# Performance work log

Hardware: AMD Instinct MI355X
Metric: run time of the kernel (lower is better)

## Reference

```python
import jax, jax.numpy as jnp
import numpy as np

B, T, D = 2, 2048, 2048
N, K, H = 16, 8, 128  # num_heads, num_kv_heads, head_dim
SOFTCAP = 50.0
ROPE_BASE = 10000.0


def apply_rope(x, positions):
    # x: [B, L, heads, H], positions: [B, L]
    head_dim = x.shape[-1]
    fraction = 2.0 * jnp.arange(head_dim // 2, dtype=jnp.float32) / head_dim
    timescale = ROPE_BASE ** fraction  # [H/2]
    sinusoid = positions.astype(jnp.float32)[..., None] / timescale  # [B, L, H/2]
    sinusoid = sinusoid[..., None, :]  # [B, L, 1, H/2]
    sin, cos = jnp.sin(sinusoid), jnp.cos(sinusoid)
    first, second = jnp.split(x, 2, axis=-1)
    out = jnp.concatenate([first * cos - second * sin,
                           second * cos + first * sin], axis=-1)
    return out.astype(x.dtype)


def setup_inputs() -> dict:
    key = jax.random.key(0)
    kx, kq, kkv, ko = jax.random.split(key, 4)
    x = jax.random.normal(kx, (B, T, D), dtype=jnp.float32)
    positions = jnp.broadcast_to(jnp.arange(T, dtype=jnp.int32), (B, T))
    attn_mask = jnp.broadcast_to(
        jnp.tril(jnp.ones((T, T), dtype=bool))[None, None], (B, 1, T, T))
    # variance-scaling fan_in init approximated with scaled normals
    w_q = jax.random.normal(kq, (N, D, H), dtype=jnp.float32) / np.sqrt(D)
    w_kv = jax.random.normal(kkv, (2, K, D, H), dtype=jnp.float32) / np.sqrt(D)
    w_out = jax.random.normal(ko, (N, H, D), dtype=jnp.float32) / np.sqrt(N * H)
    return {"x": x, "positions": positions, "attn_mask": attn_mask,
            "w_q": w_q, "w_kv": w_kv, "w_out": w_out}


def reference(x, positions, attn_mask, w_q, w_kv, w_out):
    # QKV projections (GQA: separate q and kv einsums)
    q = jnp.einsum('BTD,NDH->BTNH', x, w_q)        # [B,T,N,H]
    kv = jnp.einsum('BSD,cKDH->cBSKH', x, w_kv)     # [2,B,S,K,H]
    k, v = kv[0], kv[1]
    q = apply_rope(q, positions) * (H ** -0.5)      # rsqrt_head_dim norm
    k = apply_rope(k, positions)
    # GQA grouping: N = K * G
    G = N // K
    qg = q.reshape(B, T, K, G, H)
    logits = jnp.einsum('BTKGH,BSKH->BKGTS', qg, k).astype(jnp.float32)
    logits = jnp.tanh(logits / SOFTCAP) * SOFTCAP   # logits softcap
    big_neg = -2.3819763e+38
    masked = jnp.where(attn_mask[:, :, None, :, :], logits, big_neg)
    probs = jax.nn.softmax(masked, axis=-1).astype(k.dtype)
    encoded = jnp.einsum('BKGTS,BSKH->BTKGH', probs, v).reshape(B, T, N, H)
    return jnp.einsum('BTNH,NHD->BTD', encoded, w_out)
```

## Files before the change

### kernel.cpp

```cpp
#include <hip/hip_runtime.h>
#include <math.h>
#include <stdint.h>


typedef unsigned short u16;
using bf16x8 = __attribute__((ext_vector_type(8))) short;
using f32x4  = __attribute__((ext_vector_type(4))) float;

#define MFMA_BF16(a,b,c) __builtin_amdgcn_mfma_f32_16x16x32_bf16((a),(b),(c),0,0,0)

static __device__ __forceinline__ float b2f(u16 u) {
  union { unsigned int i; float f; } v; v.i = ((unsigned int)u) << 16; return v.f;
}
static __device__ __forceinline__ u16 f2b(float f) {
  union { float f; unsigned int i; } v; v.f = f;
  unsigned int r = v.i + 0x7fffu + ((v.i >> 16) & 1u);
  return (u16)(r >> 16);
}
static __device__ __forceinline__ unsigned pk2(float x0, float x1) {
  union { float f; unsigned u; } a, b;
  a.f = x0; b.f = x1;
  return __builtin_amdgcn_perm(b.u + 0x8000u, a.u + 0x8000u, 0x07060302u);
}
static __device__ __forceinline__ float rexp2(float a) {
  float r;
  asm("v_exp_f32 %0, %1" : "=v"(r) : "v"(a));
  return r;
}
static __device__ __forceinline__ void gload_lds16(const void* g, void* l) {
  __builtin_amdgcn_global_load_lds((__attribute__((address_space(1))) void*)(g),
                                   (__attribute__((address_space(3))) void*)(l),
                                   16, 0, 0);
}

__global__ __launch_bounds__(256) void prep(const float* __restrict__ x, u16* __restrict__ xb,
                                            const float* __restrict__ wq,
                                            const float* __restrict__ wkv,
                                            const float* __restrict__ wout,
                                            u16* __restrict__ wqkvt, u16* __restrict__ woutt) {
  const int tid = threadIdx.x;
  int bid = blockIdx.x;
  if (bid < 8192) {
    const int i = (bid * 256 + tid) * 4;
    const float4 v = *(const float4*)(x + i);
    ushort4 o;
    o.x = f2b(v.x); o.y = f2b(v.y); o.z = f2b(v.z); o.w = f2b(v.w);
    *(ushort4*)(xb + i) = o;
    return;
  }
  bid -= 8192;
  const float* src;
  u16* dst;
  int rows, cols, bx, by;
  if (bid < 8192) {
    const int seg = bid >> 12;
    const int r = bid & 4095;
    const int mat = r >> 8;
    bx = (r & 255) & 3;
    by = (r & 255) >> 2;
    rows = 2048; cols = 128;
    src = (seg ? wkv : wq) + (size_t)mat * 2048 * 128;
    dst = wqkvt + (size_t)(seg * 16 + mat) * 2048 * 128;
  } else {
    const int r = bid - 8192;
    bx = r & 63;
    by = r >> 6;
    rows = 2048; cols = 2048;
    src = wout;
    dst = woutt;
  }
  __shared__ u16 tile[32][33];
  const int c0 = bx * 32, r0 = by * 32;
  const int tx = tid & 31, ty = tid >> 5;
#pragma unroll
  for (int j = 0; j < 4; ++j)
    tile[ty + j * 8][tx] = f2b(src[(size_t)(r0 + ty + j * 8) * cols + (c0 + tx)]);
  __syncthreads();
#pragma unroll
  for (int j = 0; j < 4; ++j)
    dst[(size_t)(c0 + ty + j * 8) * rows + (r0 + tx)] = tile[tx][ty + j * 8];
}

__global__ __launch_bounds__(512, 2) void gemm_qkv(const u16* __restrict__ X,
                                                   const u16* __restrict__ wqkvt,
                                                   u16* __restrict__ qb,
                                                   u16* __restrict__ kb,
                                                   u16* __restrict__ vtb) {
  __shared__ __align__(16) u16 sAB[2][2][16384];
  const int m0 = blockIdx.x * 256;
  const int ct0 = blockIdx.y * 2;
  const u16* BT = wqkvt + (size_t)blockIdx.y * 256 * 2048;
  const int tid = threadIdx.x;
  const int wave = tid >> 6, lane = tid & 63;
  const int wm = wave >> 2, wn = wave & 3;
  const int quad = lane >> 4, l16 = lane & 15;
  const int srow = lane >> 3;
  const int sch = (lane & 7) ^ srow;

  f32x4 acc[8][4] = {};

  auto STAGE = [&](int kt, int bsel) {
    const int k0 = kt * 64;
#pragma unroll
    for (int s = 0; s < 4; ++s) {
      const int ia = wave * 4 + s;
      const int row = ia * 8 + srow;
      gload_lds16(X + (size_t)(m0 + row) * 2048 + k0 + sch * 8,
                  (char*)&sAB[bsel][0][0] + ia * 1024);
      gload_lds16(BT + (size_t)row * 2048 + k0 + sch * 8,
                  (char*)&sAB[bsel][1][0] + ia * 1024);
    }
  };

  auto COMPUTE = [&](int bsel) {
    const char* aB = (const char*)&sAB[bsel][0][0];
    const char* bB = (const char*)&sAB[bsel][1][0];
#pragma unroll
    for (int ks = 0; ks < 2; ++ks) {
      bf16x8 bfr[4];
#pragma unroll
      for (int nf = 0; nf < 4; ++nf) {
        const int Rb = wn * 64 + nf * 16 + l16;
        bfr[nf] = *(const bf16x8*)(bB + Rb * 128 + (((ks * 4 + quad) ^ (Rb & 7)) << 4));
      }
      __builtin_amdgcn_s_setprio(1);
#pragma unroll
      for (int mf = 0; mf < 8; ++mf) {
        const int R = wm * 128 + mf * 16 + l16;
        const bf16x8 af = *(const bf16x8*)(aB + R * 128 + (((ks * 4 + quad) ^ (R & 7)) << 4));
#pragma unroll
        for (int nf = 0; nf < 4; ++nf)
          acc[mf][nf] = MFMA_BF16(af, bfr[nf], acc[mf][nf]);
      }
      __builtin_amdgcn_s_setprio(0);
    }
  };

  STAGE(0, 0);
#pragma unroll 1
  for (int t = 0; t < 31; ++t) {
    STAGE(t + 1, (t + 1) & 1);
    asm volatile("s_waitcnt vmcnt(8)" ::: "memory");
    __builtin_amdgcn_s_barrier();
    asm volatile("" ::: "memory");
    COMPUTE(t & 1);
    asm volatile("" ::: "memory");
    __builtin_amdgcn_s_barrier();
    asm volatile("" ::: "memory");
  }
  asm volatile("s_waitcnt vmcnt(0)" ::: "memory");
  __builtin_amdgcn_s_barrier();
  asm volatile("" ::: "memory");
  COMPUTE(1);

#pragma unroll
  for (int mf = 0; mf < 8; ++mf) {
    const int mm = m0 + wm * 128 + mf * 16 + quad * 4;
    const int b = mm >> 11;
    const int t = mm & 2047;
#pragma unroll
    for (int nf = 0; nf < 4; ++nf) {
      const int colg = wn * 64 + nf * 16;
      const int ct = ct0 + (colg >> 7);
      const int h = (colg & 127) + l16;
      if (ct < 16) {
        u16* d = qb + (((size_t)b * 16 + ct) * 2048 + t) * 128 + h;
#pragma unroll
        for (int i = 0; i < 4; ++i) d[(size_t)i * 128] = f2b(acc[mf][nf][i]);
      } else if (ct < 24) {
        u16* d = kb + (((size_t)b * 8 + (ct - 16)) * 2048 + t) * 128 + h;
#pragma unroll
        for (int i = 0; i < 4; ++i) d[(size_t)i * 128] = f2b(acc[mf][nf][i]);
      } else {
        u16* d = vtb + (((size_t)b * 8 + (ct - 24)) * 128 + h) * 2048 + t;
        uint2 pkv;
        pkv.x = (unsigned)f2b(acc[mf][nf][0]) | ((unsigned)f2b(acc[mf][nf][1]) << 16);
        pkv.y = (unsigned)f2b(acc[mf][nf][2]) | ((unsigned)f2b(acc[mf][nf][3]) << 16);
        *(uint2*)d = pkv;
      }
    }
  }
}

__global__ __launch_bounds__(256) void rope_kernel(u16* __restrict__ qb,
                                                   u16* __restrict__ kb,
                                                   const int* __restrict__ pos) {
  const unsigned idx = blockIdx.x * 256 + threadIdx.x;
  const unsigned QP = 1u << 21;
  u16* p;
  float scale;
  int b, t, j2;
  if (idx < QP) {
    j2 = (int)(idx & 31) * 2; t = (int)((idx >> 5) & 2047);
    const int hd = (int)((idx >> 16) & 15); b = (int)(idx >> 20);
    p = qb + (((size_t)b * 16 + hd) * 2048 + t) * 128;
    scale = 0.08838834764831845f;
  } else {
    const unsigned r = idx - QP;
    j2 = (int)(r & 31) * 2; t = (int)((r >> 5) & 2047);
    const int hd = (int)((r >> 16) & 7); b = (int)(r >> 19);
    p = kb + (((size_t)b * 8 + hd) * 2048 + t) * 128;
    scale = 1.0f;
  }
  const float fpos = (float)pos[(size_t)b * 2048 + t];
  const unsigned lo = *(const unsigned*)(p + j2);
  const unsigned hi = *(const unsigned*)(p + j2 + 64);
  unsigned olo = 0, ohi = 0;
#pragma unroll
  for (int d = 0; d < 2; ++d) {
    const int j = j2 + d;
    const float ang = fpos * exp2f((float)j * -0.2076205059304601f);
    float sn, cs;
    sincosf(ang, &sn, &cs);
    const float a = b2f((u16)((d ? (lo >> 16) : lo) & 0xffffu));
    const float c2 = b2f((u16)((d ? (hi >> 16) : hi) & 0xffffu));
    olo |= ((unsigned)f2b((a * cs - c2 * sn) * scale)) << (16 * d);
    ohi |= ((unsigned)f2b((c2 * cs + a * sn) * scale)) << (16 * d);
  }
  *(unsigned*)(p + j2) = olo;
  *(unsigned*)(p + j2 + 64) = ohi;
}

__global__ __launch_bounds__(256, 4) void attn_fused(const u16* __restrict__ qg,
                                                     const u16* __restrict__ kg,
                                                     const u16* __restrict__ vtg,
                                                     u16* __restrict__ enc) {
  __shared__ __align__(16) char lds[32768];
  char* sK = lds;
  char* sV = lds + 16384;

  const int bid = blockIdx.x;
  const int half = bid >> 9;
  const int r = bid & 511;
  const int x = r & 7;
  const int g = r >> 3;
  const int pr = g & 15;
  const int head = (g >> 4) * 8 + x;
  const int Q = half ? pr : (31 - pr);
  const int b = head >> 4;
  const int n = head & 15;
  const int kh = n >> 1;

  const u16* qbase = qg + ((size_t)b * 16 + n) * 2048 * 128;
  const u16* kbase = kg + ((size_t)b * 8 + kh) * 2048 * 128;
  const u16* vbase = vtg + ((size_t)b * 8 + kh) * 128 * 2048;

  const int tid = threadIdx.x, wave = tid >> 6, lane = tid & 63;
  const int quad = lane >> 4, l16 = lane & 15;
  const int bp_a0 = ((quad & 1) * 32 + l16) * 4;
  const int bp_a1 = bp_a0 + 64;

  const float L2E = 1.4426950408889634f;
  const float C50 = 72.13475204444817f;
  const float B1 = 1.9235933879e-4f;
  const float B2 = 3.0777494206e-8f;
  const float B3 = 4.9830224200e-12f;

  const u16* kp[4];
  const u16* vp[4];
#pragma unroll
  for (int s = 0; s < 4; ++s) {
    const int kr = wave * 16 + s * 4 + quad;
    kp[s] = kbase + (size_t)kr * 128 + (l16 ^ (s * 4 + quad)) * 8;
    const int vr = wave * 32 + s * 8 + (lane >> 3);
    vp[s] = vbase + (size_t)vr * 2048 + ((lane & 7) ^ (lane >> 3)) * 8;
  }

  const int tw = Q * 64 + wave * 16;
  const int tlane = tw + l16;

  bf16x8 qf[4];
#pragma unroll
  for (int kf = 0; kf < 4; ++kf)
    qf[kf] = *(const bf16x8*)(qbase + (size_t)tlane * 128 + kf * 32 + quad * 8);

  f32x4 o[8] = {};
  f32x4 lacc = {0.f, 0.f, 0.f, 0.f};

#pragma unroll
  for (int s = 0; s < 4; ++s) {
    gload_lds16(kp[s], sK + (wave * 4 + s) * 1024);
    kp[s] += 64 * 128;
  }
#pragma unroll
  for (int s = 0; s < 4; ++s) {
    gload_lds16(vp[s], sV + (wave * 4 + s) * 1024);
    vp[s] += 64;
  }

#pragma unroll 1
  for (int si = 0; si <= Q; ++si) {
    const int s0 = si * 64;
    asm volatile("s_waitcnt vmcnt(4)" ::: "memory");
    __builtin_amdgcn_s_barrier();
    asm volatile("" ::: "memory");

    const bool diag = (si == Q);
    const int nfmax = diag ? wave : 3;
    const int kmax = diag ? (wave >> 1) : 1;

    f32x4 sacc[4];
    __builtin_amdgcn_s_setprio(1);
#pragma unroll
    for (int nf = 0; nf < 4; ++nf) {
      if (nf <= nfmax) {
        const int sr = nf * 16 + l16;
        f32x4 a = {0.f, 0.f, 0.f, 0.f};
#pragma unroll
        for (int kf = 0; kf < 4; ++kf) {
          const bf16x8 kfr =
              *(const bf16x8*)(sK + sr * 256 + (((kf * 4 + quad) ^ (sr & 15)) << 4));
          a = MFMA_BF16(kfr, qf[kf], a);
        }
        sacc[nf] = a;
      }
    }
    __builtin_amdgcn_s_setprio(0);

    asm volatile("" ::: "memory");
    __builtin_amdgcn_s_barrier();
    asm volatile("" ::: "memory");
    if (si < Q) {
#pragma unroll
      for (int s = 0; s < 4; ++s) {
        gload_lds16(kp[s], sK + (wave * 4 + s) * 1024);
        kp[s] += 64 * 128;
      }
    }

#pragma unroll
    for (int nf = 0; nf < 4; ++nf) {
      if (nf <= nfmax) {
        const f32x4 xv = sacc[nf];
        const f32x4 u = xv * xv;
        f32x4 t = u * (-B3) + B2;
        t = u * t + (-B1);
        t = u * t + L2E;
        f32x4 pv;
#pragma unroll
        for (int i = 0; i < 4; ++i) pv[i] = rexp2(fmaf(xv[i], t[i], -C50));
        if (diag) {
#pragma unroll
          for (int i = 0; i < 4; ++i) {
            const int sg = s0 + nf * 16 + quad * 4 + i;
            if (sg > tlane) pv[i] = 0.0f;
          }
        }
        sacc[nf] = pv;
        lacc += pv;
      }
    }

    unsigned pkd[4][2];
#pragma unroll
    for (int nf = 0; nf < 4; ++nf) {
      if (nf <= nfmax) {
        pkd[nf][0] = pk2(sacc[nf][0], sacc[nf][1]);
        pkd[nf][1] = pk2(sacc[nf][2], sacc[nf][3]);
      } else {
        pkd[nf][0] = 0u; pkd[nf][1] = 0u;
      }
    }

    union { int d[4]; bf16x8 v; } pb[2];
#pragma unroll
    for (int c2 = 0; c2 < 2; ++c2) {
      if (c2 <= kmax) {
        const int lo = (quad >> 1);
        const int dA0 = __builtin_amdgcn_ds_bpermute(bp_a0, (int)pkd[2 * c2][0]);
        const int dB0 = __builtin_amdgcn_ds_bpermute(bp_a0, (int)pkd[2 * c2 + 1][0]);
        const int dA1 = __builtin_amdgcn_ds_bpermute(bp_a0, (int)pkd[2 * c2][1]);
        const int dB1 = __builtin_amdgcn_ds_bpermute(bp_a0, (int)pkd[2 * c2 + 1][1]);
        const int dA2 = __builtin_amdgcn_ds_bpermute(bp_a1, (int)pkd[2 * c2][0]);
        const int dB2 = __builtin_amdgcn_ds_bpermute(bp_a1, (int)pkd[2 * c2 + 1][0]);
        const int dA3 = __builtin_amdgcn_ds_bpermute(bp_a1, (int)pkd[2 * c2][1]);
        const int dB3 = __builtin_amdgcn_ds_bpermute(bp_a1, (int)pkd[2 * c2 + 1][1]);
        pb[c2].d[0] = lo ? dB0 : dA0;
        pb[c2].d[1] = lo ? dB1 : dA1;
        pb[c2].d[2] = lo ? dB2 : dA2;
        pb[c2].d[3] = lo ? dB3 : dA3;
      }
    }

    if (si < Q) {
      asm volatile("s_waitcnt vmcnt(4)" ::: "memory");
    } else {
      asm volatile("s_waitcnt vmcnt(0)" ::: "memory");
    }
    __builtin_amdgcn_s_barrier();
    asm volatile("" ::: "memory");

#pragma unroll
    for (int c2 = 0; c2 < 2; ++c2) {
      if (c2 <= kmax) {
        __builtin_amdgcn_s_setprio(1);
#pragma unroll
        for (int nfo = 0; nfo < 8; ++nfo) {
          const int hr = nfo * 16 + l16;
          const bf16x8 vb =
              *(const bf16x8*)(sV + hr * 128 + (((c2 * 4 + quad) ^ (hr & 7)) << 4));
          o[nfo] = MFMA_BF16(vb, pb[c2].v, o[nfo]);
        }
        __builtin_amdgcn_s_setprio(0);
      }
    }

    asm volatile("" ::: "memory");
    __builtin_amdgcn_s_barrier();
    asm volatile("" ::: "memory");
    if (si < Q) {
#pragma unroll
      for (int s = 0; s < 4; ++s) {
        gload_lds16(vp[s], sV + (wave * 4 + s) * 1024);
        vp[s] += 64;
      }
    }
  }

  float lsum = lacc[0] + lacc[1] + lacc[2] + lacc[3];
  lsum += __shfl_xor(lsum, 16);
  lsum += __shfl_xor(lsum, 32);
  const float inv = 1.0f / lsum;
  u16* d = enc + (((size_t)b * 2048 + tlane) * 16 + n) * 128 + quad * 4;
#pragma unroll
  for (int nfo = 0; nfo < 8; ++nfo) {
    uint2 st;
    st.x = (unsigned)f2b(o[nfo][0] * inv) | ((unsigned)f2b(o[nfo][1] * inv) << 16);
    st.y = (unsigned)f2b(o[nfo][2] * inv) | ((unsigned)f2b(o[nfo][3] * inv) << 16);
    *(uint2*)(d + nfo * 16) = st;
  }
}

__global__ __launch_bounds__(512, 2) void gemm_out(const u16* __restrict__ A,
                                                   const u16* __restrict__ Bt,
                                                   float* __restrict__ C) {
  __shared__ __align__(16) u16 sA[2][16384];
  __shared__ __align__(16) u16 sB[2][8192];
  const int m0 = blockIdx.x * 256;
  const int n0 = blockIdx.y * 128;
  const int tid = threadIdx.x;
  const int wave = tid >> 6, lane = tid & 63;
  const int wm = wave >> 2, wn = wave & 3;
  const int quad = lane >> 4, l16 = lane & 15;
  const int srow = lane >> 3;
  const int sch = (lane & 7) ^ srow;

  f32x4 acc[8][2] = {};

  auto STAGE = [&](int kt, int bsel) {
    const int k0 = kt * 64;
#pragma unroll
    for (int s = 0; s < 4; ++s) {
      const int ia = wave * 4 + s;
      const int row = ia * 8 + srow;
      gload_lds16(A + (size_t)(m0 + row) * 2048 + k0 + sch * 8,
                  (char*)&sA[bsel][0] + ia * 1024);
    }
#pragma unroll
    for (int s = 0; s < 2; ++s) {
      const int ib = wave * 2 + s;
      const int row = ib * 8 + srow;
      gload_lds16(Bt + (size_t)(n0 + row) * 2048 + k0 + sch * 8,
                  (char*)&sB[bsel][0] + ib * 1024);
    }
  };

  auto COMPUTE = [&](int bsel) {
    const char* aB = (const char*)&sA[bsel][0];
    const char* bB = (const char*)&sB[bsel][0];
#pragma unroll
    for (int ks = 0; ks < 2; ++ks) {
      bf16x8 bfr[2];
#pragma unroll
      for (int nf = 0; nf < 2; ++nf) {
        const int Rb = wn * 32 + nf * 16 + l16;
        bfr[nf] = *(const bf16x8*)(bB + Rb * 128 + (((ks * 4 + quad) ^ (Rb & 7)) << 4));
      }
      __builtin_amdgcn_s_setprio(1);
#pragma unroll
      for (int mf = 0; mf < 8; ++mf) {
        const int R = wm * 128 + mf * 16 + l16;
        const bf16x8 af = *(const bf16x8*)(aB + R * 128 + (((ks * 4 + quad) ^ (R & 7)) << 4));
#pragma unroll
        for (int nf = 0; nf < 2; ++nf)
          acc[mf][nf] = MFMA_BF16(af, bfr[nf], acc[mf][nf]);
      }
      __builtin_amdgcn_s_setprio(0);
    }
  };

  STAGE(0, 0);
#pragma unroll 1
  for (int t = 0; t < 31; ++t) {
    STAGE(t + 1, (t + 1) & 1);
    asm volatile("s_waitcnt vmcnt(6)" ::: "memory");
    __builtin_amdgcn_s_barrier();
    asm volatile("" ::: "memory");
    COMPUTE(t & 1);
    asm volatile("" ::: "memory");
    __builtin_amdgcn_s_barrier();
    asm volatile("" ::: "memory");
  }
  asm volatile("s_waitcnt vmcnt(0)" ::: "memory");
  __builtin_amdgcn_s_barrier();
  asm volatile("" ::: "memory");
  COMPUTE(1);

#pragma unroll
  for (int mf = 0; mf < 8; ++mf) {
    const int mm = m0 + wm * 128 + mf * 16 + quad * 4;
#pragma unroll
    for (int nf = 0; nf < 2; ++nf) {
      const int col = n0 + wn * 32 + nf * 16 + l16;
#pragma unroll
      for (int i = 0; i < 4; ++i) C[(size_t)(mm + i) * 2048 + col] = acc[mf][nf][i];
    }
  }
}

extern "C" void kernel_launch(void* const* d_in, const int* in_sizes, int n_in,
                              void* d_out, int out_size, void* d_ws, size_t ws_size,
                              hipStream_t stream) {
  (void)in_sizes; (void)n_in; (void)out_size; (void)ws_size;
  const float* x     = (const float*)d_in[0];
  const int*   posi  = (const int*)d_in[1];
  const float* w_q   = (const float*)d_in[3];
  const float* w_kv  = (const float*)d_in[4];
  const float* w_out = (const float*)d_in[5];
  float* out = (float*)d_out;

  u16* ws = (u16*)d_ws;
  u16* wqkvt = ws;
  u16* woutt = ws + (size_t)8388608;
  u16* qb    = ws + (size_t)12582912;
  u16* kb    = ws + (size_t)20971520;
  u16* vtb   = ws + (size_t)25165824;
  u16* encb  = ws + (size_t)29360128;
  u16* xb    = encb;

  prep<<<20480, 256, 0, stream>>>(x, xb, w_q, w_kv, w_out, wqkvt, woutt);
  gemm_qkv<<<dim3(16, 16), 512, 0, stream>>>(xb, wqkvt, qb, kb, vtb);
  rope_kernel<<<12288, 256, 0, stream>>>(qb, kb, posi);
  attn_fused<<<1024, 256, 0, stream>>>(qb, kb, vtb, encb);
  gemm_out<<<dim3(16, 16), 512, 0, stream>>>(encb, woutt, out);
}
```

Before: 334.2 us.

## Double attention tile to 128 queries and 128 keys with 8-wave blocks

The attention kernel now uses 512-thread blocks covering 128 query rows and 128-key tiles, with 64 KB of LDS, and launches half as many blocks. Each K/V tile staged in LDS is shared by twice as many query rows, and there are half as many barrier-separated iterations per block. The softmax exponent and packing are interleaved with the QK MFMAs in two halves. In exchange it risks lower occupancy from the larger LDS and register footprint, more wasted work on the diagonal tile, and fewer blocks for load balancing.

```diff
diff --git a/kernel.cpp b/kernel.cpp
--- a/kernel.cpp
+++ b/kernel.cpp
@@ -221,22 +221,22 @@
   *(unsigned*)(p + j2 + 64) = ohi;
 }
 
-__global__ __launch_bounds__(256, 4) void attn_fused(const u16* __restrict__ qg,
+__global__ __launch_bounds__(512, 4) void attn_fused(const u16* __restrict__ qg,
                                                      const u16* __restrict__ kg,
                                                      const u16* __restrict__ vtg,
                                                      u16* __restrict__ enc) {
-  __shared__ __align__(16) char lds[32768];
+  __shared__ __align__(16) char lds[65536];
   char* sK = lds;
-  char* sV = lds + 16384;
+  char* sV = lds + 32768;
 
   const int bid = blockIdx.x;
-  const int half = bid >> 9;
-  const int r = bid & 511;
+  const int half = bid >> 8;
+  const int r = bid & 255;
   const int x = r & 7;
   const int g = r >> 3;
-  const int pr = g & 15;
-  const int head = (g >> 4) * 8 + x;
-  const int Q = half ? pr : (31 - pr);
+  const int pr = g & 7;
+  const int head = (g >> 3) * 8 + x;
+  const int Q = half ? pr : (15 - pr);
   const int b = head >> 4;
   const int n = head & 15;
   const int kh = n >> 1;
@@ -260,13 +260,13 @@
   const u16* vp[4];
 #pragma unroll
   for (int s = 0; s < 4; ++s) {
-    const int kr = wave * 16 + s * 4 + quad;
-    kp[s] = kbase + (size_t)kr * 128 + (l16 ^ (s * 4 + quad)) * 8;
-    const int vr = wave * 32 + s * 8 + (lane >> 3);
-    vp[s] = vbase + (size_t)vr * 2048 + ((lane & 7) ^ (lane >> 3)) * 8;
-  }
-
-  const int tw = Q * 64 + wave * 16;
+    const int row = wave * 16 + s * 4 + quad;
+    const int ch = l16 ^ (row & 15);
+    kp[s] = kbase + (size_t)row * 128 + ch * 8;
+    vp[s] = vbase + (size_t)row * 2048 + ch * 8;
+  }
+
+  const int tw = Q * 128 + wave * 16;
   const int tlane = tw + l16;
 
   bf16x8 qf[4];
@@ -280,42 +280,74 @@
 #pragma unroll
   for (int s = 0; s < 4; ++s) {
     gload_lds16(kp[s], sK + (wave * 4 + s) * 1024);
-    kp[s] += 64 * 128;
+    kp[s] += 128 * 128;
   }
 #pragma unroll
   for (int s = 0; s < 4; ++s) {
     gload_lds16(vp[s], sV + (wave * 4 + s) * 1024);
-    vp[s] += 64;
+    vp[s] += 128;
   }
 
 #pragma unroll 1
   for (int si = 0; si <= Q; ++si) {
-    const int s0 = si * 64;
+    const int s0 = si * 128;
     asm volatile("s_waitcnt vmcnt(4)" ::: "memory");
     __builtin_amdgcn_s_barrier();
     asm volatile("" ::: "memory");
 
     const bool diag = (si == Q);
-    const int nfmax = diag ? wave : 3;
-    const int kmax = diag ? (wave >> 1) : 1;
-
-    f32x4 sacc[4];
-    __builtin_amdgcn_s_setprio(1);
-#pragma unroll
-    for (int nf = 0; nf < 4; ++nf) {
-      if (nf <= nfmax) {
-        const int sr = nf * 16 + l16;
-        f32x4 a = {0.f, 0.f, 0.f, 0.f};
-#pragma unroll
-        for (int kf = 0; kf < 4; ++kf) {
-          const bf16x8 kfr =
-              *(const bf16x8*)(sK + sr * 256 + (((kf * 4 + quad) ^ (sr & 15)) << 4));
-          a = MFMA_BF16(kfr, qf[kf], a);
+    const int nfmax = diag ? wave : 7;
+    const int kmax = diag ? (wave >> 1) : 3;
+
+    unsigned pkd[8][2];
+#pragma unroll
+    for (int hh = 0; hh < 2; ++hh) {
+      f32x4 sacc[4];
+      __builtin_amdgcn_s_setprio(1);
+#pragma unroll
+      for (int j = 0; j < 4; ++j) {
+        const int nf = hh * 4 + j;
+        if (nf <= nfmax) {
+          const int sr = nf * 16 + l16;
+          f32x4 a = {0.f, 0.f, 0.f, 0.f};
+#pragma unroll
+          for (int kf = 0; kf < 4; ++kf) {
+            const bf16x8 kfr =
+                *(const bf16x8*)(sK + sr * 256 + (((kf * 4 + quad) ^ (sr & 15)) << 4));
+            a = MFMA_BF16(kfr, qf[kf], a);
+          }
+          sacc[j] = a;
         }
-        sacc[nf] = a;
-      }
-    }
-    __builtin_amdgcn_s_setprio(0);
+      }
+      __builtin_amdgcn_s_setprio(0);
+
+#pragma unroll
+      for (int j = 0; j < 4; ++j) {
+        const int nf = hh * 4 + j;
+        if (nf <= nfmax) {
+          const f32x4 xv = sacc[j];
+          const f32x4 u = xv * xv;
+          f32x4 t = u * (-B3) + B2;
+          t = u * t + (-B1);
+          t = u * t + L2E;
+          f32x4 pv;
+#pragma unroll
+          for (int i = 0; i < 4; ++i) pv[i] = rexp2(fmaf(xv[i], t[i], -C50));
+          if (diag) {
+#pragma unroll
+            for (int i = 0; i < 4; ++i) {
+              const int sg = s0 + nf * 16 + quad * 4 + i;
+              if (sg > tlane) pv[i] = 0.0f;
+            }
+          }
+          lacc += pv;
+          pkd[nf][0] = pk2(pv[0], pv[1]);
+          pkd[nf][1] = pk2(pv[2], pv[3]);
+        } else {
+          pkd[nf][0] = 0u; pkd[nf][1] = 0u;
+        }
+      }
+    }
 
     asm volatile("" ::: "memory");
     __builtin_amdgcn_s_barrier();
@@ -324,47 +356,20 @@
 #pragma unroll
       for (int s = 0; s < 4; ++s) {
         gload_lds16(kp[s], sK + (wave * 4 + s) * 1024);
-        kp[s] += 64 * 128;
-      }
-    }
-
-#pragma unroll
-    for (int nf = 0; nf < 4; ++nf) {
-      if (nf <= nfmax) {
-        const f32x4 xv = sacc[nf];
-        const f32x4 u = xv * xv;
-        f32x4 t = u * (-B3) + B2;
-        t = u * t + (-B1);
-        t = u * t + L2E;
-        f32x4 pv;
-#pragma unroll
-        for (int i = 0; i < 4; ++i) pv[i] = rexp2(fmaf(xv[i], t[i], -C50));
-        if (diag) {
-#pragma unroll
-          for (int i = 0; i < 4; ++i) {
-            const int sg = s0 + nf * 16 + quad * 4 + i;
-            if (sg > tlane) pv[i] = 0.0f;
-          }
-        }
-        sacc[nf] = pv;
-        lacc += pv;
-      }
-    }
-
-    unsigned pkd[4][2];
-#pragma unroll
-    for (int nf = 0; nf < 4; ++nf) {
-      if (nf <= nfmax) {
-        pkd[nf][0] = pk2(sacc[nf][0], sacc[nf][1]);
-        pkd[nf][1] = pk2(sacc[nf][2], sacc[nf][3]);
-      } else {
-        pkd[nf][0] = 0u; pkd[nf][1] = 0u;
-      }
-    }
-
-    union { int d[4]; bf16x8 v; } pb[2];
-#pragma unroll
-    for (int c2 = 0; c2 < 2; ++c2) {
+        kp[s] += 128 * 128;
+      }
+    }
+
+    if (si < Q) {
+      asm volatile("s_waitcnt vmcnt(4)" ::: "memory");
+    } else {
+      asm volatile("s_waitcnt vmcnt(0)" ::: "memory");
+    }
+    __builtin_amdgcn_s_barrier();
+    asm volatile("" ::: "memory");
+
+#pragma unroll
+    for (int c2 = 0; c2 < 4; ++c2) {
       if (c2 <= kmax) {
         const int lo = (quad >> 1);
         const int dA0 = __builtin_amdgcn_ds_bpermute(bp_a0, (int)pkd[2 * c2][0]);
@@ -375,31 +380,18 @@
         const int dB2 = __builtin_amdgcn_ds_bpermute(bp_a1, (int)pkd[2 * c2 + 1][0]);
         const int dA3 = __builtin_amdgcn_ds_bpermute(bp_a1, (int)pkd[2 * c2][1]);
         const int dB3 = __builtin_amdgcn_ds_bpermute(bp_a1, (int)pkd[2 * c2 + 1][1]);
-        pb[c2].d[0] = lo ? dB0 : dA0;
-        pb[c2].d[1] = lo ? dB1 : dA1;
-        pb[c2].d[2] = lo ? dB2 : dA2;
-        pb[c2].d[3] = lo ? dB3 : dA3;
-      }
-    }
-
-    if (si < Q) {
-      asm volatile("s_waitcnt vmcnt(4)" ::: "memory");
-    } else {
-      asm volatile("s_waitcnt vmcnt(0)" ::: "memory");
-    }
-    __builtin_amdgcn_s_barrier();
-    asm volatile("" ::: "memory");
-
-#pragma unroll
-    for (int c2 = 0; c2 < 2; ++c2) {
-      if (c2 <= kmax) {
+        union { int d[4]; bf16x8 v; } pb;
+        pb.d[0] = lo ? dB0 : dA0;
+        pb.d[1] = lo ? dB1 : dA1;
+        pb.d[2] = lo ? dB2 : dA2;
+        pb.d[3] = lo ? dB3 : dA3;
         __builtin_amdgcn_s_setprio(1);
 #pragma unroll
         for (int nfo = 0; nfo < 8; ++nfo) {
           const int hr = nfo * 16 + l16;
           const bf16x8 vb =
-              *(const bf16x8*)(sV + hr * 128 + (((c2 * 4 + quad) ^ (hr & 7)) << 4));
-          o[nfo] = MFMA_BF16(vb, pb[c2].v, o[nfo]);
+              *(const bf16x8*)(sV + hr * 256 + (((c2 * 4 + quad) ^ (hr & 15)) << 4));
+          o[nfo] = MFMA_BF16(vb, pb.v, o[nfo]);
         }
         __builtin_amdgcn_s_setprio(0);
       }
@@ -412,7 +404,7 @@
 #pragma unroll
       for (int s = 0; s < 4; ++s) {
         gload_lds16(vp[s], sV + (wave * 4 + s) * 1024);
-        vp[s] += 64;
+        vp[s] += 128;
       }
     }
   }
@@ -541,6 +533,6 @@
   prep<<<20480, 256, 0, stream>>>(x, xb, w_q, w_kv, w_out, wqkvt, woutt);
   gemm_qkv<<<dim3(16, 16), 512, 0, stream>>>(xb, wqkvt, qb, kb, vtb);
   rope_kernel<<<12288, 256, 0, stream>>>(qb, kb, posi);
-  attn_fused<<<1024, 256, 0, stream>>>(qb, kb, vtb, encb);
+  attn_fused<<<512, 512, 0, stream>>>(qb, kb, vtb, encb);
   gemm_out<<<dim3(16, 16), 512, 0, stream>>>(encb, woutt, out);
 }
```

After: 336.0 us. Within noise of the previous version (+0.6%).

## Split attention key tile across wave pairs with two query groups per wave

Applied to the files above, without the earlier changes.

Reassigns work inside the attention block so each wave handles 32 query rows (two 16-row groups) against half of the 64-key tile, rather than 16 query rows against all keys. Each loaded K and V fragment now feeds two MFMAs, which halves LDS reads per MFMA and doubles reuse. Waves whose key half lies fully above the causal diagonal skip work. Partial outputs and row sums from the two key halves are combined through LDS at the end, which adds an epilogue reduction and raises register pressure from doubled accumulators.

```diff
diff --git a/kernel.cpp b/kernel.cpp
--- a/kernel.cpp
+++ b/kernel.cpp
@@ -246,6 +246,7 @@
   const u16* vbase = vtg + ((size_t)b * 8 + kh) * 128 * 2048;
 
   const int tid = threadIdx.x, wave = tid >> 6, lane = tid & 63;
+  const int tslot = wave & 1, shalf = wave >> 1;
   const int quad = lane >> 4, l16 = lane & 15;
   const int bp_a0 = ((quad & 1) * 32 + l16) * 4;
   const int bp_a1 = bp_a0 + 64;
@@ -266,16 +267,18 @@
     vp[s] = vbase + (size_t)vr * 2048 + ((lane & 7) ^ (lane >> 3)) * 8;
   }
 
-  const int tw = Q * 64 + wave * 16;
-  const int tlane = tw + l16;
-
-  bf16x8 qf[4];
-#pragma unroll
-  for (int kf = 0; kf < 4; ++kf)
-    qf[kf] = *(const bf16x8*)(qbase + (size_t)tlane * 128 + kf * 32 + quad * 8);
-
-  f32x4 o[8] = {};
-  f32x4 lacc = {0.f, 0.f, 0.f, 0.f};
+  const int tw = Q * 64 + tslot * 32;
+
+  bf16x8 qf[2][4];
+#pragma unroll
+  for (int gg = 0; gg < 2; ++gg)
+#pragma unroll
+    for (int kf = 0; kf < 4; ++kf)
+      qf[gg][kf] = *(const bf16x8*)(qbase + (size_t)(tw + gg * 16 + l16) * 128 + kf * 32 + quad * 8);
+
+  f32x4 o[2][8] = {};
+  f32x4 lacc0 = {0.f, 0.f, 0.f, 0.f};
+  f32x4 lacc1 = {0.f, 0.f, 0.f, 0.f};
 
 #pragma unroll
   for (int s = 0; s < 4; ++s) {
@@ -290,32 +293,35 @@
 
 #pragma unroll 1
   for (int si = 0; si <= Q; ++si) {
-    const int s0 = si * 64;
+    const int s0w = si * 64 + shalf * 32;
+    const int dl = tw + 31 - s0w;
+    const bool live = dl >= 0;
+    const bool dodiag = (s0w + 31 > tw);
+
     asm volatile("s_waitcnt vmcnt(4)" ::: "memory");
     __builtin_amdgcn_s_barrier();
     asm volatile("" ::: "memory");
 
-    const bool diag = (si == Q);
-    const int nfmax = diag ? wave : 3;
-    const int kmax = diag ? (wave >> 1) : 1;
-
-    f32x4 sacc[4];
-    __builtin_amdgcn_s_setprio(1);
-#pragma unroll
-    for (int nf = 0; nf < 4; ++nf) {
-      if (nf <= nfmax) {
-        const int sr = nf * 16 + l16;
-        f32x4 a = {0.f, 0.f, 0.f, 0.f};
+    f32x4 sa[2][2];
+    if (live) {
+      __builtin_amdgcn_s_setprio(1);
+#pragma unroll
+      for (int nf = 0; nf < 2; ++nf) {
+        const int sr = shalf * 32 + nf * 16 + l16;
+        f32x4 a0 = {0.f, 0.f, 0.f, 0.f};
+        f32x4 a1 = {0.f, 0.f, 0.f, 0.f};
 #pragma unroll
         for (int kf = 0; kf < 4; ++kf) {
           const bf16x8 kfr =
               *(const bf16x8*)(sK + sr * 256 + (((kf * 4 + quad) ^ (sr & 15)) << 4));
-          a = MFMA_BF16(kfr, qf[kf], a);
+          a0 = MFMA_BF16(kfr, qf[0][kf], a0);
+          a1 = MFMA_BF16(kfr, qf[1][kf], a1);
         }
-        sacc[nf] = a;
-      }
-    }
-    __builtin_amdgcn_s_setprio(0);
+        sa[nf][0] = a0;
+        sa[nf][1] = a1;
+      }
+      __builtin_amdgcn_s_setprio(0);
+    }
 
     asm volatile("" ::: "memory");
     __builtin_amdgcn_s_barrier();
@@ -328,57 +334,52 @@
       }
     }
 
-#pragma unroll
-    for (int nf = 0; nf < 4; ++nf) {
-      if (nf <= nfmax) {
-        const f32x4 xv = sacc[nf];
-        const f32x4 u = xv * xv;
-        f32x4 t = u * (-B3) + B2;
-        t = u * t + (-B1);
-        t = u * t + L2E;
-        f32x4 pv;
-#pragma unroll
-        for (int i = 0; i < 4; ++i) pv[i] = rexp2(fmaf(xv[i], t[i], -C50));
-        if (diag) {
-#pragma unroll
-          for (int i = 0; i < 4; ++i) {
-            const int sg = s0 + nf * 16 + quad * 4 + i;
-            if (sg > tlane) pv[i] = 0.0f;
+    unsigned pkd[2][2][2];
+    if (live) {
+#pragma unroll
+      for (int nf = 0; nf < 2; ++nf) {
+#pragma unroll
+        for (int gg = 0; gg < 2; ++gg) {
+          const f32x4 xv = sa[nf][gg];
+          const f32x4 u = xv * xv;
+          f32x4 t = u * (-B3) + B2;
+          t = u * t + (-B1);
+          t = u * t + L2E;
+          f32x4 pv;
+#pragma unroll
+          for (int i = 0; i < 4; ++i) pv[i] = rexp2(fmaf(xv[i], t[i], -C50));
+          if (dodiag) {
+            const int tl = tw + gg * 16 + l16;
+#pragma unroll
+            for (int i = 0; i < 4; ++i) {
+              const int sg = s0w + nf * 16 + quad * 4 + i;
+              if (sg > tl) pv[i] = 0.0f;
+            }
           }
+          if (gg == 0) lacc0 += pv; else lacc1 += pv;
+          pkd[gg][nf][0] = pk2(pv[0], pv[1]);
+          pkd[gg][nf][1] = pk2(pv[2], pv[3]);
         }
-        sacc[nf] = pv;
-        lacc += pv;
-      }
-    }
-
-    unsigned pkd[4][2];
-#pragma unroll
-    for (int nf = 0; nf < 4; ++nf) {
-      if (nf <= nfmax) {
-        pkd[nf][0] = pk2(sacc[nf][0], sacc[nf][1]);
-        pkd[nf][1] = pk2(sacc[nf][2], sacc[nf][3]);
-      } else {
-        pkd[nf][0] = 0u; pkd[nf][1] = 0u;
       }
     }
 
     union { int d[4]; bf16x8 v; } pb[2];
-#pragma unroll
-    for (int c2 = 0; c2 < 2; ++c2) {
-      if (c2 <= kmax) {
-        const int lo = (quad >> 1);
-        const int dA0 = __builtin_amdgcn_ds_bpermute(bp_a0, (int)pkd[2 * c2][0]);
-        const int dB0 = __builtin_amdgcn_ds_bpermute(bp_a0, (int)pkd[2 * c2 + 1][0]);
-        const int dA1 = __builtin_amdgcn_ds_bpermute(bp_a0, (int)pkd[2 * c2][1]);
-        const int dB1 = __builtin_amdgcn_ds_bpermute(bp_a0, (int)pkd[2 * c2 + 1][1]);
-        const int dA2 = __builtin_amdgcn_ds_bpermute(bp_a1, (int)pkd[2 * c2][0]);
-        const int dB2 = __builtin_amdgcn_ds_bpermute(bp_a1, (int)pkd[2 * c2 + 1][0]);
-        const int dA3 = __builtin_amdgcn_ds_bpermute(bp_a1, (int)pkd[2 * c2][1]);
-        const int dB3 = __builtin_amdgcn_ds_bpermute(bp_a1, (int)pkd[2 * c2 + 1][1]);
-        pb[c2].d[0] = lo ? dB0 : dA0;
-        pb[c2].d[1] = lo ? dB1 : dA1;
-        pb[c2].d[2] = lo ? dB2 : dA2;
-        pb[c2].d[3] = lo ? dB3 : dA3;
+    if (live) {
+      const int lo = (quad >> 1);
+#pragma unroll
+      for (int gg = 0; gg < 2; ++gg) {
+        const int dA0 = __builtin_amdgcn_ds_bpermute(bp_a0, (int)pkd[gg][0][0]);
+        const int dB0 = __builtin_amdgcn_ds_bpermute(bp_a0, (int)pkd[gg][1][0]);
+        const int dA1 = __builtin_amdgcn_ds_bpermute(bp_a0, (int)pkd[gg][0][1]);
+        const int dB1 = __builtin_amdgcn_ds_bpermute(bp_a0, (int)pkd[gg][1][1]);
+        const int dA2 = __builtin_amdgcn_ds_bpermute(bp_a1, (int)pkd[gg][0][0]);
+        const int dB2 = __builtin_amdgcn_ds_bpermute(bp_a1, (int)pkd[gg][1][0]);
+        const int dA3 = __builtin_amdgcn_ds_bpermute(bp_a1, (int)pkd[gg][0][1]);
+        const int dB3 = __builtin_amdgcn_ds_bpermute(bp_a1, (int)pkd[gg][1][1]);
+        pb[gg].d[0] = lo ? dB0 : dA0;
+        pb[gg].d[1] = lo ? dB1 : dA1;
+        pb[gg].d[2] = lo ? dB2 : dA2;
+        pb[gg].d[3] = lo ? dB3 : dA3;
       }
     }
 
@@ -390,19 +391,17 @@
     __builtin_amdgcn_s_barrier();
     asm volatile("" ::: "memory");
 
-#pragma unroll
-    for (int c2 = 0; c2 < 2; ++c2) {
-      if (c2 <= kmax) {
-        __builtin_amdgcn_s_setprio(1);
-#pragma unroll
-        for (int nfo = 0; nfo < 8; ++nfo) {
-          const int hr = nfo * 16 + l16;
-          const bf16x8 vb =
-              *(const bf16x8*)(sV + hr * 128 + (((c2 * 4 + quad) ^ (hr & 7)) << 4));
-          o[nfo] = MFMA_BF16(vb, pb[c2].v, o[nfo]);
-        }
-        __builtin_amdgcn_s_setprio(0);
-      }
+    if (live) {
+      __builtin_amdgcn_s_setprio(1);
+#pragma unroll
+      for (int nfo = 0; nfo < 8; ++nfo) {
+        const int hr = nfo * 16 + l16;
+        const bf16x8 vb =
+            *(const bf16x8*)(sV + hr * 128 + (((shalf * 4 + quad) ^ (hr & 7)) << 4));
+        o[0][nfo] = MFMA_BF16(vb, pb[0].v, o[0][nfo]);
+        o[1][nfo] = MFMA_BF16(vb, pb[1].v, o[1][nfo]);
+      }
+      __builtin_amdgcn_s_setprio(0);
     }
 
     asm volatile("" ::: "memory");
@@ -417,17 +416,46 @@
     }
   }
 
-  float lsum = lacc[0] + lacc[1] + lacc[2] + lacc[3];
-  lsum += __shfl_xor(lsum, 16);
-  lsum += __shfl_xor(lsum, 32);
-  const float inv = 1.0f / lsum;
-  u16* d = enc + (((size_t)b * 2048 + tlane) * 16 + n) * 128 + quad * 4;
-#pragma unroll
-  for (int nfo = 0; nfo < 8; ++nfo) {
-    uint2 st;
-    st.x = (unsigned)f2b(o[nfo][0] * inv) | ((unsigned)f2b(o[nfo][1] * inv) << 16);
-    st.y = (unsigned)f2b(o[nfo][2] * inv) | ((unsigned)f2b(o[nfo][3] * inv) << 16);
-    *(uint2*)(d + nfo * 16) = st;
+  float lsum0 = lacc0[0] + lacc0[1] + lacc0[2] + lacc0[3];
+  lsum0 += __shfl_xor(lsum0, 16); lsum0 += __shfl_xor(lsum0, 32);
+  float lsum1 = lacc1[0] + lacc1[1] + lacc1[2] + lacc1[3];
+  lsum1 += __shfl_xor(lsum1, 16); lsum1 += __shfl_xor(lsum1, 32);
+
+  float* red = (float*)lds;
+  __syncthreads();
+  if (lane < 16) {
+    red[(wave * 2 + 0) * 16 + lane] = lsum0;
+    red[(wave * 2 + 1) * 16 + lane] = lsum1;
+  }
+  __syncthreads();
+  const int pw = wave ^ 2;
+  lsum0 += red[(pw * 2 + 0) * 16 + l16];
+  lsum1 += red[(pw * 2 + 1) * 16 + l16];
+  __syncthreads();
+  if (shalf) {
+#pragma unroll
+    for (int gg = 0; gg < 2; ++gg)
+#pragma unroll
+      for (int nfo = 0; nfo < 8; ++nfo)
+        *(f32x4*)(lds + (((tslot * 2 + gg) * 8 + nfo) * 1024) + lane * 16) = o[gg][nfo];
+  }
+  __syncthreads();
+  if (!shalf) {
+#pragma unroll
+    for (int gg = 0; gg < 2; ++gg) {
+      const float inv = 1.0f / (gg ? lsum1 : lsum0);
+      const int tlg = tw + gg * 16 + l16;
+      u16* d = enc + (((size_t)b * 2048 + tlg) * 16 + n) * 128 + quad * 4;
+#pragma unroll
+      for (int nfo = 0; nfo < 8; ++nfo) {
+        f32x4 ov = o[gg][nfo];
+        ov += *(const f32x4*)(lds + (((tslot * 2 + gg) * 8 + nfo) * 1024) + lane * 16);
+        uint2 st;
+        st.x = (unsigned)f2b(ov[0] * inv) | ((unsigned)f2b(ov[1] * inv) << 16);
+        st.y = (unsigned)f2b(ov[2] * inv) | ((unsigned)f2b(ov[3] * inv) << 16);
+        *(uint2*)(d + nfo * 16) = st;
+      }
+    }
   }
 }
 
```

Measured after the change: 637.8 us. 90.8% more time.
